# Optimization experiments

Hardware: AMD Instinct MI355X
Metric: run time of the kernel (lower is better)

The kernel has to match this reference:

```python
import jax, jax.numpy as jnp
import numpy as np

B, S, HID = 2, 2048, 2048
H, HKV, D = 16, 4, 128        # num_heads, num_kv_heads, head_dim
G = H // HKV                   # GQA group size
CLIP = 8.0                     # clip_qkv
THETA = 10000.0                # rope_theta_within_seq
N_SEQS = 8                     # max_num_sequences


def setup_inputs() -> dict:
    key = jax.random.key(0)
    ks = jax.random.split(key, 6)
    hidden_states = jax.random.normal(ks[0], (B, S, HID), dtype=jnp.float32)
    within_seq_position_ids = jnp.broadcast_to(jnp.arange(S, dtype=jnp.int64), (B, S))
    global_position_ids = jnp.broadcast_to(jnp.arange(S, dtype=jnp.int64), (B, S))
    sequence_ids = jnp.sort(jax.random.randint(ks[1], (B, S), 0, N_SEQS, dtype=jnp.int64), axis=-1)
    scale = 0.02
    Wq = jax.random.normal(ks[2], (H * D, HID), dtype=jnp.float32) * scale
    Wk = jax.random.normal(ks[3], (HKV * D, HID), dtype=jnp.float32) * scale
    Wv = jax.random.normal(ks[4], (HKV * D, HID), dtype=jnp.float32) * scale
    Wo = jax.random.normal(ks[5], (HID, H * D), dtype=jnp.float32) * scale
    return {"hidden_states": hidden_states,
            "within_seq_position_ids": within_seq_position_ids,
            "global_position_ids": global_position_ids,
            "sequence_ids": sequence_ids,
            "Wq": Wq, "Wk": Wk, "Wv": Wv, "Wo": Wo}


def _rotate_half(x):
    x1, x2 = jnp.split(x, 2, axis=-1)
    return jnp.concatenate((-x2, x1), axis=-1)


def _rope_cos_sin(position_ids, dtype):
    # inv_freq: [D/2]
    inv_freq = THETA ** (-(jnp.arange(0, D, 2, dtype=jnp.float32) / D))
    angles = position_ids.astype(jnp.float32)[..., None] * inv_freq  # [B,S,D/2]
    angles = jnp.concatenate((angles, angles), axis=-1)              # [B,S,D]
    # unsqueeze head dim -> [B,S,1,D]
    return jnp.cos(angles)[:, :, None, :].astype(dtype), jnp.sin(angles)[:, :, None, :].astype(dtype)


def reference(hidden_states, within_seq_position_ids, global_position_ids, sequence_ids, Wq, Wk, Wv, Wo):
    b, s, _ = hidden_states.shape
    q = (hidden_states @ Wq.T).reshape(b, s, H, D)
    k = (hidden_states @ Wk.T).reshape(b, s, HKV, D)
    v = (hidden_states @ Wv.T).reshape(b, s, HKV, D)
    # clip_qkv
    q = jnp.clip(q, -CLIP, CLIP)
    k = jnp.clip(k, -CLIP, CLIP)
    v = jnp.clip(v, -CLIP, CLIP)
    # RoPE (within_seq layer -> within_seq_position_ids)
    cos, sin = _rope_cos_sin(within_seq_position_ids, q.dtype)
    q = q * cos + _rotate_half(q) * sin
    k = k * cos + _rotate_half(k) * sin
    # GQA: group queries by kv head instead of materializing repeat_kv
    q = q.transpose(0, 2, 1, 3).reshape(b, HKV, G, s, D)  # [B,HKV,G,S,D]
    k = k.transpose(0, 2, 1, 3)                            # [B,HKV,S,D]
    v = v.transpose(0, 2, 1, 3)
    scores = jnp.einsum('bhgqd,bhkd->bhgqk', q, k) / jnp.sqrt(jnp.asarray(D, q.dtype))
    # block-diagonal (same sequence) causal mask
    qi = jnp.arange(s)
    causal = qi[:, None] >= qi[None, :]                    # [S,S]
    same_seq = sequence_ids[:, :, None] == sequence_ids[:, None, :]  # [B,S,S]
    mask = (causal[None] & same_seq)[:, None, None, :, :]  # [B,1,1,S,S]
    scores = jnp.where(mask, scores, jnp.finfo(scores.dtype).min)
    attn = jax.nn.softmax(scores, axis=-1)
    out = jnp.einsum('bhgqk,bhkd->bhgqd', attn, v)         # [B,HKV,G,S,D]
    out = out.reshape(b, H, s, D).transpose(0, 2, 1, 3).reshape(b, s, H * D)
    return out @ Wo.T
```

## Files before the change

kernel.cpp:

```cpp
#include <hip/hip_runtime.h>
#include <hip/hip_bf16.h>

typedef __hip_bfloat16 bf16;
typedef __attribute__((ext_vector_type(8))) short bf16x8;
typedef __attribute__((ext_vector_type(4))) float f32x4;

#define MFMA_BF16(a, b, c) __builtin_amdgcn_mfma_f32_16x16x32_bf16((a), (b), (c), 0, 0, 0)

#define B_   2
#define S_   2048
#define HID_ 2048
#define H_   16
#define HKV_ 4
#define D_   128

#define GLOAD_LDS(gptr, lptr) \
  __builtin_amdgcn_global_load_lds((const __attribute__((address_space(1))) void*)(gptr), \
                                   (__attribute__((address_space(3))) void*)(lptr), 16, 0, 0)

template <int N>
__device__ __forceinline__ void vmw() {
  if constexpr (N == 0)      asm volatile("s_waitcnt vmcnt(0)" ::: "memory");
  else if constexpr (N == 4) asm volatile("s_waitcnt vmcnt(4)" ::: "memory");
  else if constexpr (N == 5) asm volatile("s_waitcnt vmcnt(5)" ::: "memory");
  else                       asm volatile("s_waitcnt vmcnt(6)" ::: "memory");
}

__device__ __forceinline__ void blk_barrier() {
  __builtin_amdgcn_sched_barrier(0);
  __builtin_amdgcn_s_barrier();
  __builtin_amdgcn_sched_barrier(0);
}

__global__ void cvt_all(const float* __restrict__ hidden, const float* __restrict__ Wq,
                        const float* __restrict__ Wk, const float* __restrict__ Wv,
                        const float* __restrict__ Wo,
                        bf16* __restrict__ Xb, bf16* __restrict__ Wqkv, bf16* __restrict__ Wob) {
  long long i4 = (long long)blockIdx.x * 256 + threadIdx.x;
  const float* src; bf16* dst; long long off;
  if (i4 < 2097152)      { src = hidden; dst = Xb;             off = i4; }
  else if (i4 < 3145728) { src = Wq;     dst = Wqkv;           off = i4 - 2097152; }
  else if (i4 < 3407872) { src = Wk;     dst = Wqkv + 4194304; off = i4 - 3145728; }
  else if (i4 < 3670016) { src = Wv;     dst = Wqkv + 5242880; off = i4 - 3407872; }
  else                   { src = Wo;     dst = Wob;            off = i4 - 3670016; }
  float4 v = *reinterpret_cast<const float4*>(src + off * 4);
  alignas(8) bf16 t[4];
  t[0] = __float2bfloat16(v.x);
  t[1] = __float2bfloat16(v.y);
  t[2] = __float2bfloat16(v.z);
  t[3] = __float2bfloat16(v.w);
  *reinterpret_cast<short4*>(dst + off * 4) = *reinterpret_cast<const short4*>(t);
}

__global__ void seq_start(const int* __restrict__ seq, int* __restrict__ sstart) {
  int t = blockIdx.x * 256 + threadIdx.x;
  int b = t >> 11, s = t & (S_ - 1);
  const int* sb = seq + b * S_;
  int sid = sb[s];
  int lo = 0, hi = s;
  while (lo < hi) {
    int mid = (lo + hi) >> 1;
    if (sb[mid] < sid) lo = mid + 1; else hi = mid;
  }
  sstart[t] = lo;
}

template <int BM, int BN, int OUT_BF16>
__global__ __launch_bounds__(512, 2) void gemm8p(const bf16* __restrict__ A,
                                                 const bf16* __restrict__ Bw,
                                                 void* __restrict__ Cout,
                                                 int M, int N, int K) {
  constexpr int MR = BM / 32;
  constexpr int NR = BN / 64;
  constexpr int LA = BM / 128;
  constexpr int QD = NR + 2;

  __shared__ bf16 As[2][2][BM * 32];
  __shared__ bf16 Bs[2][BN * 64];

  const int tid  = threadIdx.x;
  const int lane = tid & 63;
  const int w    = tid >> 6;
  const int wr   = w >> 2;
  const int wc   = w & 3;
  const int ln15 = lane & 15, g = lane >> 4;

  const int nwg = gridDim.x;
  int bid = blockIdx.x;
  bid = (bid & 7) * (nwg >> 3) + (bid >> 3);
  const int nbn = N / BN;
  const int m0 = (bid / nbn) * BM;
  const int n0 = (bid % nbn) * BN;

  f32x4 acc[MR][NR] = {};

  auto stageA = [&](int db, int kh, int t) {
    int kc = t * 64 + kh * 32;
#pragma unroll
    for (int r = 0; r < LA; r++) {
      int sIdx = r * 512 + tid;
      int row = sIdx >> 2;
      int ss = (sIdx & 3) ^ ((row >> 1) & 3);
      GLOAD_LDS(A + (size_t)(m0 + row) * K + kc + ss * 8, &As[db][kh][(r * 512 + w * 64) * 8]);
    }
  };
  auto stageB = [&](int db, int t) {
#pragma unroll
    for (int r = 0; r < NR; r++) {
      int sIdx = r * 512 + tid;
      int row = sIdx >> 3;
      int cs = (sIdx & 7) ^ (row & 7);
      GLOAD_LDS(Bw + (size_t)(n0 + row) * K + t * 64 + cs * 8, &Bs[db][(size_t)(r * 512 + w * 64) * 8]);
    }
  };

  bf16x8 af[4], bfr[NR];
  auto rdA = [&](int db, int kh, int mb) {
#pragma unroll
    for (int m = 0; m < 4; m++) {
      int row = wr * (BM / 2) + (mb + m) * 16 + ln15;
      af[m] = *reinterpret_cast<const bf16x8*>(&As[db][kh][row * 32 + ((g ^ ((row >> 1) & 3)) << 3)]);
    }
  };
  auto rdB = [&](int db, int kh) {
#pragma unroll
    for (int n = 0; n < NR; n++) {
      int row = wc * (BN / 4) + n * 16 + ln15;
      int sl = ((kh << 2) + g) ^ (row & 7);
      bfr[n] = *reinterpret_cast<const bf16x8*>(&Bs[db][row * 64 + sl * 8]);
    }
  };
  auto MF = [&](int mb) {
    __builtin_amdgcn_s_setprio(1);
#pragma unroll
    for (int m = 0; m < 4; m++)
#pragma unroll
      for (int n = 0; n < NR; n++)
        acc[mb + m][n] = MFMA_BF16(af[m], bfr[n], acc[mb + m][n]);
    __builtin_amdgcn_s_setprio(0);
  };

  const int NT = K >> 6;

  stageA(0, 0, 0);
  stageA(0, 1, 0);
  stageB(0, 0);
  stageA(1, 0, 1);
  stageB(1, 1);
  vmw<QD>();
  blk_barrier();

  for (int T = 0; T < NT; ++T) {
    const int db = T & 1, dn = db ^ 1;

    rdA(db, 0, 0); rdB(db, 0);
    if (T + 1 < NT) stageA(dn, 1, T + 1);
    MF(0); blk_barrier();

    rdA(db, 0, 4);
    MF(4); blk_barrier();

    rdA(db, 1, 0); rdB(db, 1);
    if (T + 2 < NT) stageA(db, 0, T + 2);
    MF(0); blk_barrier();

    rdA(db, 1, 4);
    if (T + 2 < NT) stageB(db, T + 2);
    MF(4);
    if (T + 1 < NT) {
      if (T == NT - 2) vmw<0>(); else vmw<QD>();
    }
    blk_barrier();
  }

#pragma unroll
  for (int m = 0; m < MR; m++)
#pragma unroll
    for (int n = 0; n < NR; n++)
#pragma unroll
      for (int r = 0; r < 4; r++) {
        int row = m0 + wr * (BM / 2) + m * 16 + g * 4 + r;
        int col = n0 + wc * (BN / 4) + n * 16 + ln15;
        if constexpr (OUT_BF16) {
          ((bf16*)Cout)[(size_t)row * N + col] = __float2bfloat16(acc[m][n][r]);
        } else {
          ((float*)Cout)[(size_t)row * N + col] = acc[m][n][r];
        }
      }
}

__global__ __launch_bounds__(256) void qkv_post(const bf16* __restrict__ QKV,
                                                const int* __restrict__ wpos,
                                                bf16* __restrict__ Qs,
                                                bf16* __restrict__ Ks) {
  const int row = blockIdx.x;
  const int b = row >> 11, s = row & (S_ - 1);
  const int t = threadIdx.x;
  const bf16* R = QKV + (size_t)row * 3072;
  const float pos = (float)wpos[row];
  const float kln = 0.14391156831212787f;
  const float qscale = 0.08838834764831845f;

  for (int p = t; p < 1024; p += 256) {
    int h = p >> 6, i = p & 63;
    float ang = pos * expf(-(float)i * kln);
    float sn, cs;
    sincosf(ang, &sn, &cs);
    float x1 = __bfloat162float(R[h * 128 + i]);
    float x2 = __bfloat162float(R[h * 128 + 64 + i]);
    x1 = fminf(fmaxf(x1, -8.f), 8.f);
    x2 = fminf(fmaxf(x2, -8.f), 8.f);
    float y1 = (x1 * cs - x2 * sn) * qscale;
    float y2 = (x2 * cs + x1 * sn) * qscale;
    size_t qb = ((size_t)(b * H_ + h) * S_ + s) * D_;
    Qs[qb + i]      = __float2bfloat16(y1);
    Qs[qb + 64 + i] = __float2bfloat16(y2);
  }
  {
    int kh = t >> 6, i = t & 63;
    float ang = pos * expf(-(float)i * kln);
    float sn, cs;
    sincosf(ang, &sn, &cs);
    float x1 = __bfloat162float(R[2048 + kh * 128 + i]);
    float x2 = __bfloat162float(R[2048 + kh * 128 + 64 + i]);
    x1 = fminf(fmaxf(x1, -8.f), 8.f);
    x2 = fminf(fmaxf(x2, -8.f), 8.f);
    float y1 = x1 * cs - x2 * sn;
    float y2 = x2 * cs + x1 * sn;
    size_t kb = ((size_t)(b * HKV_ + kh) * S_ + s) * D_;
    Ks[kb + i]      = __float2bfloat16(y1);
    Ks[kb + 64 + i] = __float2bfloat16(y2);
  }
}

__global__ __launch_bounds__(256) void vt_trans(const bf16* __restrict__ QKV,
                                                bf16* __restrict__ Vt) {
  __shared__ bf16 Tl[64][132];
  const int t = threadIdx.x;
  const int blk = blockIdx.x;
  const int st = blk & 31, kvh = (blk >> 5) & 3, b = blk >> 7;
  const int s0 = st * 64;

#pragma unroll
  for (int p = 0; p < 8; p++) {
    int r = p * 8 + (t >> 5);
    int c = (t & 31) * 4;
    short4 v = *reinterpret_cast<const short4*>(QKV + (size_t)(b * S_ + s0 + r) * 3072 + 2560 + kvh * 128 + c);
    alignas(8) bf16 e[4];
    *reinterpret_cast<short4*>(e) = v;
#pragma unroll
    for (int k = 0; k < 4; k++) {
      float x = __bfloat162float(e[k]);
      x = fminf(fmaxf(x, -8.f), 8.f);
      Tl[r][c + k] = __float2bfloat16(x);
    }
  }
  __syncthreads();

  if (t < 128) {
    const int d = t;
    bf16* dst = Vt + ((size_t)(b * HKV_ + kvh) * D_ + d) * S_ + s0;
#pragma unroll
    for (int j = 0; j < 64; j += 8) {
      alignas(16) bf16 v[8];
#pragma unroll
      for (int k = 0; k < 8; k++) v[k] = Tl[j + k][d];
      *reinterpret_cast<short4*>(dst + j)     = *reinterpret_cast<const short4*>(&v[0]);
      *reinterpret_cast<short4*>(dst + j + 4) = *reinterpret_cast<const short4*>(&v[4]);
    }
  }
}

__global__ __launch_bounds__(256) void attn_fwd(const bf16* __restrict__ Qs,
                                                const bf16* __restrict__ Ks,
                                                const bf16* __restrict__ Vt,
                                                const int* __restrict__ sstart,
                                                bf16* __restrict__ att) {
  __shared__ bf16 Kl[2][32 * 128];
  __shared__ bf16 Vl[2][128 * 32];
  __shared__ bf16 Plds[4][2][16 * 32];

  const int tid = threadIdx.x;
  const int lane = tid & 63, w = tid >> 6;
  const int ln15 = lane & 15, g = lane >> 4;

  const int wg = ((blockIdx.x & 7) << 6) | (blockIdx.x >> 3);
  const int qt  = wg & 63;
  const int kvh = (wg >> 6) & 3;
  const int b   = wg >> 8;
  const int h   = kvh * 4 + w;
  const int q0  = qt * 32;
  const int qa  = q0 + ln15;
  const int qb  = q0 + 16 + ln15;

  const bf16* Qbase = Qs + (size_t)(b * H_ + h) * S_ * D_;
  bf16x8 qfa[4], qfb[4];
#pragma unroll
  for (int c = 0; c < 4; c++) {
    qfa[c] = *reinterpret_cast<const bf16x8*>(Qbase + (size_t)qa * D_ + c * 32 + g * 8);
    qfb[c] = *reinterpret_cast<const bf16x8*>(Qbase + (size_t)qb * D_ + c * 32 + g * 8);
  }

  const int sQa = sstart[b * S_ + qa];
  const int sQb = sstart[b * S_ + qb];
  const int kstart = __builtin_amdgcn_readfirstlane(__shfl(sQa, 0));
  const int kend = q0 + 31;

  const bf16* Kb = Ks + (size_t)(b * HKV_ + kvh) * S_ * D_;
  const bf16* Vb = Vt + (size_t)(b * HKV_ + kvh) * D_ * S_;

  auto stage = [&](int buf, int kb) {
#pragma unroll
    for (int p = 0; p < 2; p++) {
      int slot = p * 256 + tid;
      int row = slot >> 4;
      int cs = (slot & 15) ^ (row & 15);
      int gr = min(kb + row, S_ - 1);
      GLOAD_LDS(Kb + (size_t)gr * D_ + cs * 8, &Kl[buf][(p * 256 + w * 64) * 8]);
    }
#pragma unroll
    for (int p = 0; p < 2; p++) {
      int slot = p * 256 + tid;
      int d = slot >> 2, c = slot & 3;
      int cs = c ^ (d & 3);
      int gcol = min(kb + cs * 8, S_ - 8);
      GLOAD_LDS(Vb + (size_t)d * S_ + gcol, &Vl[buf][(p * 256 + w * 64) * 8]);
    }
  };

  float ma = -1e30f, la = 0.f, mb = -1e30f, lb = 0.f;
  f32x4 oa[8] = {}, ob[8] = {};

  auto softmax = [&](const f32x4& s0, const f32x4& s1, int qi, int sQ, int kb,
                     float& m, float& lsum, f32x4 (&o)[8], bf16* pdst) {
    float sc[8];
    float tmax = -1e30f;
#pragma unroll
    for (int r = 0; r < 4; r++) {
      int k0i = kb + g * 4 + r;
      int k1i = k0i + 16;
      float x0 = (k0i >= sQ && k0i <= qi) ? s0[r] : -1e30f;
      float x1 = (k1i >= sQ && k1i <= qi) ? s1[r] : -1e30f;
      sc[r] = x0;
      sc[4 + r] = x1;
      tmax = fmaxf(tmax, fmaxf(x0, x1));
    }
    tmax = fmaxf(tmax, __shfl_xor(tmax, 16));
    tmax = fmaxf(tmax, __shfl_xor(tmax, 32));
    float mn  = fmaxf(m, tmax);
    float fac = __expf(m - mn);
    float ps = 0.f;
    alignas(16) bf16 pb[8];
#pragma unroll
    for (int i2 = 0; i2 < 8; i2++) {
      float p = (sc[i2] < -1e29f) ? 0.f : __expf(sc[i2] - mn);
      ps += p;
      pb[i2] = __float2bfloat16(p);
    }
    ps += __shfl_xor(ps, 16);
    ps += __shfl_xor(ps, 32);
    lsum = lsum * fac + ps;
    m = mn;
#pragma unroll
    for (int t2 = 0; t2 < 8; t2++) o[t2] *= fac;
    *reinterpret_cast<short4*>(pdst + ln15 * 32 + g * 4)      = *reinterpret_cast<const short4*>(&pb[0]);
    *reinterpret_cast<short4*>(pdst + ln15 * 32 + 16 + g * 4) = *reinterpret_cast<const short4*>(&pb[4]);
  };

  stage(0, kstart);
  int buf = 0;
  for (int kb = kstart; kb <= kend; kb += 32) {
    __syncthreads();
    if (kb + 32 <= kend) stage(buf ^ 1, kb + 32);

    bf16x8 kf0[4], kf1[4];
#pragma unroll
    for (int c = 0; c < 4; c++) {
      kf0[c] = *reinterpret_cast<const bf16x8*>(&Kl[buf][ln15 * 128 + (((c * 4 + g) ^ ln15) << 3)]);
      kf1[c] = *reinterpret_cast<const bf16x8*>(&Kl[buf][(16 + ln15) * 128 + (((c * 4 + g) ^ ln15) << 3)]);
    }
    f32x4 sa0 = {0.f, 0.f, 0.f, 0.f}, sa1 = sa0, sb0 = sa0, sb1 = sa0;
#pragma unroll
    for (int c = 0; c < 4; c++) {
      sa0 = MFMA_BF16(kf0[c], qfa[c], sa0);
      sa1 = MFMA_BF16(kf1[c], qfa[c], sa1);
      sb0 = MFMA_BF16(kf0[c], qfb[c], sb0);
      sb1 = MFMA_BF16(kf1[c], qfb[c], sb1);
    }

    softmax(sa0, sa1, qa, sQa, kb, ma, la, oa, &Plds[w][0][0]);
    softmax(sb0, sb1, qb, sQb, kb, mb, lb, ob, &Plds[w][1][0]);
    __builtin_amdgcn_wave_barrier();
    bf16x8 pfa = *reinterpret_cast<const bf16x8*>(&Plds[w][0][ln15 * 32 + g * 8]);
    bf16x8 pfb = *reinterpret_cast<const bf16x8*>(&Plds[w][1][ln15 * 32 + g * 8]);

#pragma unroll
    for (int t2 = 0; t2 < 8; t2++) {
      int d = t2 * 16 + ln15;
      bf16x8 vf = *reinterpret_cast<const bf16x8*>(&Vl[buf][d * 32 + ((g ^ (ln15 & 3)) << 3)]);
      oa[t2] = MFMA_BF16(vf, pfa, oa[t2]);
      ob[t2] = MFMA_BF16(vf, pfb, ob[t2]);
    }
    __builtin_amdgcn_wave_barrier();
    buf ^= 1;
  }

  float inva = 1.f / la;
  float invb = 1.f / lb;
#pragma unroll
  for (int t2 = 0; t2 < 8; t2++)
#pragma unroll
    for (int r = 0; r < 4; r++) {
      int d = t2 * 16 + g * 4 + r;
      att[((size_t)(b * S_ + qa)) * (H_ * D_) + h * D_ + d] = __float2bfloat16(oa[t2][r] * inva);
      att[((size_t)(b * S_ + qb)) * (H_ * D_) + h * D_ + d] = __float2bfloat16(ob[t2][r] * invb);
    }
}

extern "C" void kernel_launch(void* const* d_in, const int* in_sizes, int n_in,
                              void* d_out, int out_size, void* d_ws, size_t ws_size,
                              hipStream_t stream) {
  const float* hidden = (const float*)d_in[0];
  const int* wpos = (const int*)d_in[1];
  const int* seq = (const int*)d_in[3];
  const float* Wq = (const float*)d_in[4];
  const float* Wk = (const float*)d_in[5];
  const float* Wv = (const float*)d_in[6];
  const float* Wo = (const float*)d_in[7];

  char* ws = (char*)d_ws;
  bf16* Xb   = (bf16*)(ws);
  bf16* Wqkv = (bf16*)(ws + 16777216);
  bf16* Wob  = (bf16*)(ws + 29360128);
  bf16* QKVb = (bf16*)(ws + 37748736);
  bf16* Ksb  = (bf16*)(ws + 62914560);
  bf16* Vtb  = (bf16*)(ws + 67108864);
  int*  sst  = (int*)(ws + 71303168);
  bf16* Qsb  = Xb;
  bf16* attb = QKVb;

  cvt_all<<<dim3(18432), dim3(256), 0, stream>>>(hidden, Wq, Wk, Wv, Wo, Xb, Wqkv, Wob);
  seq_start<<<dim3(32), dim3(256), 0, stream>>>(seq, sst);

  gemm8p<256, 192, 1><<<dim3(256), dim3(512), 0, stream>>>(Xb, Wqkv, (void*)QKVb, 4096, 3072, 2048);

  qkv_post<<<dim3(4096), dim3(256), 0, stream>>>(QKVb, wpos, Qsb, Ksb);
  vt_trans<<<dim3(256), dim3(256), 0, stream>>>(QKVb, Vtb);

  attn_fwd<<<dim3(512), dim3(256), 0, stream>>>(Qsb, Ksb, Vtb, sst, attb);

  gemm8p<256, 128, 0><<<dim3(256), dim3(512), 0, stream>>>(attb, Wob, d_out, 4096, 2048, 2048);
}
```

Baseline: 166.2 us.

## Ping-pong register fragments in GEMM main loop and reshape output-projection tile

```diff
diff --git a/kernel.cpp b/kernel.cpp
--- a/kernel.cpp
+++ b/kernel.cpp
@@ -21,6 +21,8 @@
 template <int N>
 __device__ __forceinline__ void vmw() {
   if constexpr (N == 0)      asm volatile("s_waitcnt vmcnt(0)" ::: "memory");
+  else if constexpr (N == 1) asm volatile("s_waitcnt vmcnt(1)" ::: "memory");
+  else if constexpr (N == 2) asm volatile("s_waitcnt vmcnt(2)" ::: "memory");
   else if constexpr (N == 4) asm volatile("s_waitcnt vmcnt(4)" ::: "memory");
   else if constexpr (N == 5) asm volatile("s_waitcnt vmcnt(5)" ::: "memory");
   else                       asm volatile("s_waitcnt vmcnt(6)" ::: "memory");
@@ -71,9 +73,10 @@
                                                  void* __restrict__ Cout,
                                                  int M, int N, int K) {
   constexpr int MR = BM / 32;
+  constexpr int MH = MR / 2;
   constexpr int NR = BN / 64;
   constexpr int LA = BM / 128;
-  constexpr int QD = NR + 2;
+  constexpr int QD = LA + NR;
 
   __shared__ bf16 As[2][2][BM * 32];
   __shared__ bf16 Bs[2][BN * 64];
@@ -114,29 +117,30 @@
     }
   };
 
-  bf16x8 af[4], bfr[NR];
-  auto rdA = [&](int db, int kh, int mb) {
-#pragma unroll
-    for (int m = 0; m < 4; m++) {
-      int row = wr * (BM / 2) + (mb + m) * 16 + ln15;
-      af[m] = *reinterpret_cast<const bf16x8*>(&As[db][kh][row * 32 + ((g ^ ((row >> 1) & 3)) << 3)]);
-    }
-  };
-  auto rdB = [&](int db, int kh) {
+  bf16x8 afA[MH], afB[MH], bfE[NR], bfO[NR];
+
+  auto rdA = [&](bf16x8 (&dst)[MH], int db, int kh, int mh) {
+#pragma unroll
+    for (int m = 0; m < MH; m++) {
+      int row = wr * (BM / 2) + (mh * MH + m) * 16 + ln15;
+      dst[m] = *reinterpret_cast<const bf16x8*>(&As[db][kh][row * 32 + ((g ^ ((row >> 1) & 3)) << 3)]);
+    }
+  };
+  auto rdB = [&](bf16x8 (&dst)[NR], int db, int kh) {
 #pragma unroll
     for (int n = 0; n < NR; n++) {
       int row = wc * (BN / 4) + n * 16 + ln15;
       int sl = ((kh << 2) + g) ^ (row & 7);
-      bfr[n] = *reinterpret_cast<const bf16x8*>(&Bs[db][row * 64 + sl * 8]);
-    }
-  };
-  auto MF = [&](int mb) {
+      dst[n] = *reinterpret_cast<const bf16x8*>(&Bs[db][row * 64 + sl * 8]);
+    }
+  };
+  auto MF = [&](bf16x8 (&Af)[MH], bf16x8 (&Bf)[NR], int mh) {
     __builtin_amdgcn_s_setprio(1);
 #pragma unroll
-    for (int m = 0; m < 4; m++)
+    for (int m = 0; m < MH; m++)
 #pragma unroll
       for (int n = 0; n < NR; n++)
-        acc[mb + m][n] = MFMA_BF16(af[m], bfr[n], acc[mb + m][n]);
+        acc[mh * MH + m][n] = MFMA_BF16(Af[m], Bf[n], acc[mh * MH + m][n]);
     __builtin_amdgcn_s_setprio(0);
   };
 
@@ -149,28 +153,29 @@
   stageB(1, 1);
   vmw<QD>();
   blk_barrier();
+  rdA(afA, 0, 0, 0);
+  rdB(bfE, 0, 0);
 
   for (int T = 0; T < NT; ++T) {
     const int db = T & 1, dn = db ^ 1;
 
-    rdA(db, 0, 0); rdB(db, 0);
+    rdA(afB, db, 0, 1);
     if (T + 1 < NT) stageA(dn, 1, T + 1);
-    MF(0); blk_barrier();
-
-    rdA(db, 0, 4);
-    MF(4); blk_barrier();
-
-    rdA(db, 1, 0); rdB(db, 1);
+    MF(afA, bfE, 0); blk_barrier();
+
+    rdA(afA, db, 1, 0); rdB(bfO, db, 1);
+    MF(afB, bfE, 1); blk_barrier();
+
+    rdA(afB, db, 1, 1);
     if (T + 2 < NT) stageA(db, 0, T + 2);
-    MF(0); blk_barrier();
-
-    rdA(db, 1, 4);
+    MF(afA, bfO, 0);
+    if (T + 2 < NT) vmw<LA>();
+    else if (T + 1 < NT) vmw<0>();
+    blk_barrier();
+
+    if (T + 1 < NT) { rdA(afA, dn, 0, 0); rdB(bfE, dn, 0); }
     if (T + 2 < NT) stageB(db, T + 2);
-    MF(4);
-    if (T + 1 < NT) {
-      if (T == NT - 2) vmw<0>(); else vmw<QD>();
-    }
-    blk_barrier();
+    MF(afB, bfO, 1); blk_barrier();
   }
 
 #pragma unroll
@@ -449,5 +454,5 @@
 
   attn_fwd<<<dim3(512), dim3(256), 0, stream>>>(Qsb, Ksb, Vtb, sst, attb);
 
-  gemm8p<256, 128, 0><<<dim3(256), dim3(512), 0, stream>>>(attb, Wob, d_out, 4096, 2048, 2048);
-}
+  gemm8p<128, 256, 0><<<dim3(256), dim3(512), 0, stream>>>(attb, Wob, d_out, 4096, 2048, 2048);
+}
```

New measurement: 170.1 us. 2.4% more time.

## Restructure GEMM pipeline with single-buffered A, shallower prefetch, and higher occupancy

Applied to the files above, without the earlier changes.

```diff
diff --git a/kernel.cpp b/kernel.cpp
--- a/kernel.cpp
+++ b/kernel.cpp
@@ -21,8 +21,8 @@
 template <int N>
 __device__ __forceinline__ void vmw() {
   if constexpr (N == 0)      asm volatile("s_waitcnt vmcnt(0)" ::: "memory");
+  else if constexpr (N == 3) asm volatile("s_waitcnt vmcnt(3)" ::: "memory");
   else if constexpr (N == 4) asm volatile("s_waitcnt vmcnt(4)" ::: "memory");
-  else if constexpr (N == 5) asm volatile("s_waitcnt vmcnt(5)" ::: "memory");
   else                       asm volatile("s_waitcnt vmcnt(6)" ::: "memory");
 }
 
@@ -66,16 +66,16 @@
 }
 
 template <int BM, int BN, int OUT_BF16>
-__global__ __launch_bounds__(512, 2) void gemm8p(const bf16* __restrict__ A,
+__global__ __launch_bounds__(512, 4) void gemm8p(const bf16* __restrict__ A,
                                                  const bf16* __restrict__ Bw,
                                                  void* __restrict__ Cout,
                                                  int M, int N, int K) {
   constexpr int MR = BM / 32;
+  constexpr int MH = MR / 2;
   constexpr int NR = BN / 64;
   constexpr int LA = BM / 128;
-  constexpr int QD = NR + 2;
-
-  __shared__ bf16 As[2][2][BM * 32];
+
+  __shared__ bf16 As[2][BM * 32];
   __shared__ bf16 Bs[2][BN * 64];
 
   const int tid  = threadIdx.x;
@@ -94,14 +94,14 @@
 
   f32x4 acc[MR][NR] = {};
 
-  auto stageA = [&](int db, int kh, int t) {
+  auto stageA = [&](int kh, int t) {
     int kc = t * 64 + kh * 32;
 #pragma unroll
     for (int r = 0; r < LA; r++) {
       int sIdx = r * 512 + tid;
       int row = sIdx >> 2;
       int ss = (sIdx & 3) ^ ((row >> 1) & 3);
-      GLOAD_LDS(A + (size_t)(m0 + row) * K + kc + ss * 8, &As[db][kh][(r * 512 + w * 64) * 8]);
+      GLOAD_LDS(A + (size_t)(m0 + row) * K + kc + ss * 8, &As[kh][(r * 512 + w * 64) * 8]);
     }
   };
   auto stageB = [&](int db, int t) {
@@ -114,12 +114,12 @@
     }
   };
 
-  bf16x8 af[4], bfr[NR];
-  auto rdA = [&](int db, int kh, int mb) {
-#pragma unroll
-    for (int m = 0; m < 4; m++) {
-      int row = wr * (BM / 2) + (mb + m) * 16 + ln15;
-      af[m] = *reinterpret_cast<const bf16x8*>(&As[db][kh][row * 32 + ((g ^ ((row >> 1) & 3)) << 3)]);
+  bf16x8 af[MH], bfr[NR];
+  auto rdA = [&](int kh, int mh) {
+#pragma unroll
+    for (int m = 0; m < MH; m++) {
+      int row = wr * (BM / 2) + (mh * MH + m) * 16 + ln15;
+      af[m] = *reinterpret_cast<const bf16x8*>(&As[kh][row * 32 + ((g ^ ((row >> 1) & 3)) << 3)]);
     }
   };
   auto rdB = [&](int db, int kh) {
@@ -130,46 +130,42 @@
       bfr[n] = *reinterpret_cast<const bf16x8*>(&Bs[db][row * 64 + sl * 8]);
     }
   };
-  auto MF = [&](int mb) {
+  auto MF = [&](int mh) {
     __builtin_amdgcn_s_setprio(1);
 #pragma unroll
-    for (int m = 0; m < 4; m++)
+    for (int m = 0; m < MH; m++)
 #pragma unroll
       for (int n = 0; n < NR; n++)
-        acc[mb + m][n] = MFMA_BF16(af[m], bfr[n], acc[mb + m][n]);
+        acc[mh * MH + m][n] = MFMA_BF16(af[m], bfr[n], acc[mh * MH + m][n]);
     __builtin_amdgcn_s_setprio(0);
   };
 
   const int NT = K >> 6;
 
-  stageA(0, 0, 0);
-  stageA(0, 1, 0);
+  stageA(0, 0);
   stageB(0, 0);
-  stageA(1, 0, 1);
-  stageB(1, 1);
-  vmw<QD>();
+  vmw<0>();
   blk_barrier();
 
   for (int T = 0; T < NT; ++T) {
     const int db = T & 1, dn = db ^ 1;
 
-    rdA(db, 0, 0); rdB(db, 0);
-    if (T + 1 < NT) stageA(dn, 1, T + 1);
+    rdA(0, 0); rdB(db, 0);
+    stageA(1, T);
     MF(0); blk_barrier();
 
-    rdA(db, 0, 4);
-    MF(4); blk_barrier();
-
-    rdA(db, 1, 0); rdB(db, 1);
-    if (T + 2 < NT) stageA(db, 0, T + 2);
+    rdA(0, 1);
+    if (T + 1 < NT) stageB(dn, T + 1);
+    MF(1); blk_barrier();
+
+    if (T + 1 < NT) vmw<NR>(); else vmw<0>();
+    rdA(1, 0); rdB(db, 1);
+    if (T + 1 < NT) stageA(0, T + 1);
     MF(0); blk_barrier();
 
-    rdA(db, 1, 4);
-    if (T + 2 < NT) stageB(db, T + 2);
-    MF(4);
-    if (T + 1 < NT) {
-      if (T == NT - 2) vmw<0>(); else vmw<QD>();
-    }
+    rdA(1, 1);
+    MF(1);
+    if (T + 1 < NT) vmw<0>();
     blk_barrier();
   }
 
@@ -449,5 +445,5 @@
 
   attn_fwd<<<dim3(512), dim3(256), 0, stream>>>(Qsb, Ksb, Vtb, sst, attb);
 
-  gemm8p<256, 128, 0><<<dim3(256), dim3(512), 0, stream>>>(attb, Wob, d_out, 4096, 2048, 2048);
-}
+  gemm8p<128, 256, 0><<<dim3(256), dim3(512), 0, stream>>>(attb, Wob, d_out, 4096, 2048, 2048);
+}
```

Result: slower. 249.1 us (+49.9%).
